# Kernel optimization log

Hardware: AMD Instinct MI355X
Metric: run time of the kernel (lower is better)

Reference implementation:

```python
import jax, jax.numpy as jnp
import numpy as np

B, T, F, H, P, HEADS = 1024, 128, 9, 256, 2048, 4
DH = H // HEADS

def _lstm_layer(x, Wih, Whh, bih, bhh):
    # x: [B,T,in]; gate order i,f,g,o (torch convention)
    xp = jnp.einsum('bti,gi->btg', x, Wih) + bih + bhh  # [B,T,4H]
    h0 = jnp.zeros((x.shape[0], Whh.shape[1]), x.dtype)
    def step(carry, xt):
        h, c = carry
        g = xt + h @ Whh.T
        i, f, gg, o = jnp.split(g, 4, axis=-1)
        c = jax.nn.sigmoid(f) * c + jax.nn.sigmoid(i) * jnp.tanh(gg)
        h = jax.nn.sigmoid(o) * jnp.tanh(c)
        return (h, c), h
    _, hs = jax.lax.scan(step, (h0, h0), jnp.swapaxes(xp, 0, 1))
    return jnp.swapaxes(hs, 0, 1)  # [B,T,H]

def _layernorm(x, g, b, eps=1e-5):
    mu = x.mean(-1, keepdims=True)
    var = ((x - mu) ** 2).mean(-1, keepdims=True)
    return (x - mu) * jax.lax.rsqrt(var + eps) * g + b

def setup_inputs():
    key = jax.random.key(0)
    ks = jax.random.split(key, 30)
    w = lambda k, s: jax.random.normal(k, s, jnp.float32) * 0.05
    return {
        'x': jax.random.normal(ks[0], (B, T, F), jnp.float32),
        'sku_indices': jnp.arange(B, dtype=jnp.int32),
        'adj': jax.random.uniform(ks[1], (P, P), jnp.float32),
        'vsn_emb_w': w(ks[2], (F, H)), 'vsn_emb_b': w(ks[3], (F, H)),
        'vsn_sel_w': w(ks[4], (F, F)), 'vsn_sel_b': w(ks[5], (F,)),
        'lstm_Wih0': w(ks[6], (4 * H, H)), 'lstm_Whh0': w(ks[7], (4 * H, H)),
        'lstm_bih0': w(ks[8], (4 * H,)), 'lstm_bhh0': w(ks[9], (4 * H,)),
        'lstm_Wih1': w(ks[10], (4 * H, H)), 'lstm_Whh1': w(ks[11], (4 * H, H)),
        'lstm_bih1': w(ks[12], (4 * H,)), 'lstm_bhh1': w(ks[13], (4 * H,)),
        'attn_in_w': w(ks[14], (3 * H, H)), 'attn_in_b': w(ks[15], (3 * H,)),
        'attn_out_w': w(ks[16], (H, H)), 'attn_out_b': w(ks[17], (H,)),
        'gnn_w': w(ks[18], (H, H)), 'gnn_b': w(ks[19], (H,)),
        'ln_g': jnp.ones((H,), jnp.float32), 'ln_b': jnp.zeros((H,), jnp.float32),
        'gate_w': w(ks[20], (H, 2 * H)), 'gate_b': w(ks[21], (H,)),
        'out_w': w(ks[22], (1, H)), 'out_b': w(ks[23], (1,)),
    }

def reference(x, sku_indices, adj, vsn_emb_w, vsn_emb_b, vsn_sel_w, vsn_sel_b,
              lstm_Wih0, lstm_Whh0, lstm_bih0, lstm_bhh0,
              lstm_Wih1, lstm_Whh1, lstm_bih1, lstm_bhh1,
              attn_in_w, attn_in_b, attn_out_w, attn_out_b,
              gnn_w, gnn_b, ln_g, ln_b, gate_w, gate_b, out_w, out_b):
    # --- TFT hidden: variable selection -> 2-layer LSTM -> MHA, take last step ---
    emb = x[..., None] * vsn_emb_w + vsn_emb_b           # [B,T,F,H]
    wts = jax.nn.softmax(x @ vsn_sel_w.T + vsn_sel_b, -1)  # [B,T,F]
    h = jnp.einsum('btf,btfh->bth', wts, emb)            # [B,T,H]
    h = _lstm_layer(h, lstm_Wih0, lstm_Whh0, lstm_bih0, lstm_bhh0)
    h = _lstm_layer(h, lstm_Wih1, lstm_Whh1, lstm_bih1, lstm_bhh1)
    qkv = h @ attn_in_w.T + attn_in_b                    # [B,T,3H]
    q, k, v = [a.reshape(B, T, HEADS, DH) for a in jnp.split(qkv, 3, axis=-1)]
    scores = jnp.einsum('bqhd,bkhd->bhqk', q, k) / np.sqrt(DH).astype(np.float32)
    attn = jax.nn.softmax(scores, -1)
    o = jnp.einsum('bhqk,bkhd->bqhd', attn, v).reshape(B, T, H)
    o = o @ attn_out_w.T + attn_out_b
    hidden = o[:, -1, :]                                  # [B,H]
    # --- GNN enrichment (all sku_indices valid here) ---
    product_embeds = jnp.zeros((P, H), hidden.dtype).at[sku_indices].set(hidden)
    degree = jnp.clip(adj.sum(1, keepdims=True), 1e-6)
    aggregated = (adj / degree) @ product_embeds          # [P,H]
    transformed = jax.nn.gelu(aggregated @ gnn_w.T + gnn_b, approximate=False)
    transformed = _layernorm(transformed, ln_g, ln_b)
    enriched = transformed[sku_indices]                   # [B,H]
    gate = jax.nn.sigmoid(jnp.concatenate([hidden, enriched], -1) @ gate_w.T + gate_b)
    combined = gate * enriched + (1.0 - gate) * hidden
    out = combined @ out_w.T + out_b                      # [B,1]
    return out.squeeze(-1)
```

## Files before the change

### kernel.cpp

```cpp
#include <hip/hip_runtime.h>
#include <hip/hip_fp16.h>

typedef _Float16 f16;
typedef _Float16 f16x8 __attribute__((ext_vector_type(8)));
typedef _Float16 f16x4 __attribute__((ext_vector_type(4)));
typedef float f32x4 __attribute__((ext_vector_type(4)));

#define B_ 1024
#define T_ 128
#define F_ 9
#define H_ 256
#define P_ 2048

#define AL(p) __hip_atomic_load((p), __ATOMIC_RELAXED, __HIP_MEMORY_SCOPE_AGENT)
#define AS(p, v) __hip_atomic_store((p), (v), __ATOMIC_RELAXED, __HIP_MEMORY_SCOPE_AGENT)

__device__ __forceinline__ float sigf(float x) { return 1.f / (1.f + __expf(-x)); }
__device__ __forceinline__ float tanh_(float x) {
  float a = fminf(fabsf(x), 12.f);
  float e = __expf(2.f * a);
  float r = 1.f - 2.f / (e + 1.f);
  return copysignf(r, x);
}

__device__ __forceinline__ f16x8 aload16(const f16* p) {
  union { unsigned long long u[2]; f16x8 v; } r;
  r.u[0] = AL((const unsigned long long*)p);
  r.u[1] = AL((const unsigned long long*)p + 1);
  return r.v;
}

__device__ __forceinline__ float blk_sum(float v) {
  __shared__ float sh[8];
  int lane = threadIdx.x & 63, w = threadIdx.x >> 6;
  int nw = blockDim.x >> 6;
#pragma unroll
  for (int o = 32; o > 0; o >>= 1) v += __shfl_xor(v, o, 64);
  __syncthreads();
  if (lane == 0) sh[w] = v;
  __syncthreads();
  float t = 0.f;
  for (int i = 0; i < nw; i++) t += sh[i];
  return t;
}

__global__ __launch_bounds__(256) void gemm_f16(
    const f16* __restrict__ A, int lda,
    const f16* __restrict__ Bt, int ldb,
    const float* __restrict__ bias,
    f16* __restrict__ o16, int ldo16,
    float* __restrict__ o32, int ldo32,
    int M, int N, int K)
{
  __shared__ __align__(16) f16 As[128][40];
  __shared__ __align__(16) f16 Bs[128][40];
  const int tid = threadIdx.x;
  const int lane = tid & 63, wave = tid >> 6;
  const int wr = (wave >> 1) * 64, wc = (wave & 1) * 64;
  const int q = lane >> 4, l15 = lane & 15;
  const int bm = blockIdx.x * 128, bn = blockIdx.y * 128;

  f32x4 acc[4][4];
#pragma unroll
  for (int i = 0; i < 4; i++)
#pragma unroll
    for (int j = 0; j < 4; j++) acc[i][j] = (f32x4){0.f, 0.f, 0.f, 0.f};

  for (int k0 = 0; k0 < K; k0 += 32) {
#pragma unroll
    for (int c = 0; c < 2; ++c) {
      int ch = tid + c * 256;
      int row = ch >> 2, kh = (ch & 3) * 8;
      *(f16x8*)&As[row][kh] = *(const f16x8*)&A[(size_t)(bm + row) * lda + k0 + kh];
      *(f16x8*)&Bs[row][kh] = *(const f16x8*)&Bt[(size_t)(bn + row) * ldb + k0 + kh];
    }
    __syncthreads();
    f16x8 af[4], bf[4];
#pragma unroll
    for (int tm = 0; tm < 4; tm++) af[tm] = *(const f16x8*)&As[wr + tm * 16 + l15][q * 8];
#pragma unroll
    for (int tn = 0; tn < 4; tn++) bf[tn] = *(const f16x8*)&Bs[wc + tn * 16 + l15][q * 8];
#pragma unroll
    for (int tm = 0; tm < 4; tm++)
#pragma unroll
      for (int tn = 0; tn < 4; tn++)
        acc[tm][tn] = __builtin_amdgcn_mfma_f32_16x16x32_f16(af[tm], bf[tn], acc[tm][tn], 0, 0, 0);
    __syncthreads();
  }
#pragma unroll
  for (int tm = 0; tm < 4; tm++) {
#pragma unroll
    for (int tn = 0; tn < 4; tn++) {
      int colg = bn + wc + tn * 16 + l15;
      float bv = bias ? bias[colg] : 0.f;
#pragma unroll
      for (int r = 0; r < 4; r++) {
        int rowg = bm + wr + tm * 16 + q * 4 + r;
        float v = acc[tm][tn][r] + bv;
        if (o32) o32[(size_t)rowg * ldo32 + colg] = v;
        if (o16) o16[(size_t)rowg * ldo16 + colg] = (f16)v;
      }
    }
  }
}

__global__ __launch_bounds__(256, 1) void lstm_pipe(
    f16* __restrict__ hio,
    const f16* __restrict__ wpk0, const f16* __restrict__ wpk1,
    const float* __restrict__ b0, const float* __restrict__ b1,
    int* __restrict__ cnt0, int* __restrict__ cnt1)
{
  __shared__ __align__(16) f16 apf[2][16][64][8];
  __shared__ __align__(16) f16 htile[32][64];
  const int tid = threadIdx.x;
  const int lane = tid & 63, w = tid >> 6;
  const int q = lane >> 4, l15 = lane & 15;
  const int layer = blockIdx.x >> 7;
  const int lbid = blockIdx.x & 127;
  const int grp = lbid & 31, s = lbid >> 5;
  const int m0 = grp * 32;
  const f16* wpk = layer ? wpk1 : wpk0;
  const float* bias = layer ? b1 : b0;
  int* myflags = (layer ? cnt1 : cnt0) + grp * 64;
  int* xflags  = cnt0 + grp * 64;

  const int own0 = ((w >> 1) == s);
  const int own1 = (((w + 4) >> 1) == s);
  const int offh = (w & 1) * 32;

  f16x8 bf[4][16];
  {
    const f16* wbase = wpk + (((size_t)(s * 4 + w) * 4) * 16) * 512 + lane * 8;
#pragma unroll
    for (int g = 0; g < 4; g++)
#pragma unroll
      for (int k = 0; k < 16; k++)
        bf[g][k] = *(const f16x8*)(wbase + (size_t)(g * 16 + k) * 512);
  }
  float bv[4];
#pragma unroll
  for (int g = 0; g < 4; g++) bv[g] = bias[g * 256 + s * 64 + w * 16 + l15];

  const int srow = lane & 15, scb = lane >> 4;
  size_t rb[2];
  rb[0] = ((size_t)(m0 + srow) * T_) * 256 + scb * 8;
  rb[1] = ((size_t)(m0 + 16 + srow) * T_) * 256 + scb * 8;

  const f16x8 zv = {(f16)0, (f16)0, (f16)0, (f16)0, (f16)0, (f16)0, (f16)0, (f16)0};

  if (layer) {
    if (tid == 0) {
      int it = 0;
      for (;;) {
        unsigned long long a = AL((unsigned long long*)xflags);
        unsigned long long b2 = AL((unsigned long long*)xflags + 1);
        if ((int)a >= 2 && (int)(a >> 32) >= 2 &&
            (int)b2 >= 2 && (int)(b2 >> 32) >= 2) break;
        __builtin_amdgcn_s_sleep(1);
        if (++it > (1 << 22)) break;
      }
    }
    __syncthreads();
  }
  f16x8 xr[2][2];
#pragma unroll
  for (int mt = 0; mt < 2; mt++) {
    if (layer) {
      xr[mt][0] = aload16(&hio[rb[mt] + (size_t)w * 32]);
      xr[mt][1] = aload16(&hio[rb[mt] + (size_t)(w + 4) * 32]);
    } else {
      xr[mt][0] = *(const f16x8*)&hio[rb[mt] + (size_t)w * 32];
      xr[mt][1] = *(const f16x8*)&hio[rb[mt] + (size_t)(w + 4) * 32];
    }
  }
  float cst[2][4] = {{0.f, 0.f, 0.f, 0.f}, {0.f, 0.f, 0.f, 0.f}};

  __syncthreads();
  if (tid == 0) AS(&myflags[s], 1);

  for (int t = 0; t < T_; ++t) {
    if (tid == 0) {
      const int needO = t + 1;
      int needX = 0;
      if (layer) { needX = t + 3; if (needX > T_ + 1) needX = T_ + 1; }
      int it = 0;
      for (;;) {
        unsigned long long a = AL((unsigned long long*)myflags);
        unsigned long long b2 = AL((unsigned long long*)myflags + 1);
        bool ok = (int)a >= needO && (int)(a >> 32) >= needO &&
                  (int)b2 >= needO && (int)(b2 >> 32) >= needO;
        if (ok && layer) {
          unsigned long long c = AL((unsigned long long*)xflags);
          unsigned long long d = AL((unsigned long long*)xflags + 1);
          ok = (int)c >= needX && (int)(c >> 32) >= needX &&
               (int)d >= needX && (int)(d >> 32) >= needX;
        }
        if (ok) break;
        __builtin_amdgcn_s_sleep(1);
        if (++it > (1 << 22)) break;
      }
    }
    __syncthreads();

#pragma unroll
    for (int mt = 0; mt < 2; mt++) {
      *(f16x8*)&apf[mt][w][lane][0]     = xr[mt][0];
      *(f16x8*)&apf[mt][w + 4][lane][0] = xr[mt][1];
      f16x8 h0 = zv, h1 = zv;
      if (t > 0) {
        if (own0) h0 = *(const f16x8*)&htile[mt * 16 + srow][offh + scb * 8];
        else      h0 = aload16(&hio[rb[mt] + (size_t)(t - 1) * 256 + (size_t)w * 32]);
        if (own1) h1 = *(const f16x8*)&htile[mt * 16 + srow][offh + scb * 8];
        else      h1 = aload16(&hio[rb[mt] + (size_t)(t - 1) * 256 + (size_t)(w + 4) * 32]);
      }
      *(f16x8*)&apf[mt][8 + w][lane][0]  = h0;
      *(f16x8*)&apf[mt][12 + w][lane][0] = h1;
    }
    __syncthreads();

    f32x4 acc[2][4];
#pragma unroll
    for (int mt = 0; mt < 2; mt++)
#pragma unroll
      for (int g = 0; g < 4; g++) acc[mt][g] = (f32x4){0.f, 0.f, 0.f, 0.f};
#pragma unroll
    for (int k = 0; k < 16; k++) {
      f16x8 a0 = *(const f16x8*)&apf[0][k][lane][0];
      f16x8 a1 = *(const f16x8*)&apf[1][k][lane][0];
#pragma unroll
      for (int g = 0; g < 4; g++) {
        acc[0][g] = __builtin_amdgcn_mfma_f32_16x16x32_f16(a0, bf[g][k], acc[0][g], 0, 0, 0);
        acc[1][g] = __builtin_amdgcn_mfma_f32_16x16x32_f16(a1, bf[g][k], acc[1][g], 0, 0, 0);
      }
    }
    if (t + 1 < T_) {
#pragma unroll
      for (int mt = 0; mt < 2; mt++) {
        if (layer) {
          xr[mt][0] = aload16(&hio[rb[mt] + (size_t)(t + 1) * 256 + (size_t)w * 32]);
          xr[mt][1] = aload16(&hio[rb[mt] + (size_t)(t + 1) * 256 + (size_t)(w + 4) * 32]);
        } else {
          xr[mt][0] = *(const f16x8*)&hio[rb[mt] + (size_t)(t + 1) * 256 + (size_t)w * 32];
          xr[mt][1] = *(const f16x8*)&hio[rb[mt] + (size_t)(t + 1) * 256 + (size_t)(w + 4) * 32];
        }
      }
    }
    f16 hn[2][4];
#pragma unroll
    for (int mt = 0; mt < 2; mt++)
#pragma unroll
      for (int r = 0; r < 4; r++) {
        float ip = acc[mt][0][r] + bv[0];
        float fp = acc[mt][1][r] + bv[1];
        float gp = acc[mt][2][r] + bv[2];
        float op = acc[mt][3][r] + bv[3];
        float cn = sigf(fp) * cst[mt][r] + sigf(ip) * tanh_(gp);
        cst[mt][r] = cn;
        hn[mt][r] = (f16)(sigf(op) * tanh_(cn));
      }
#pragma unroll
    for (int mt = 0; mt < 2; mt++)
#pragma unroll
      for (int r = 0; r < 4; r++)
        htile[mt * 16 + q * 4 + r][w * 16 + l15] = hn[mt][r];
    __syncthreads();
    {
      int row = tid >> 3, c8 = (tid & 7) * 8;
      union { unsigned long long u[2]; f16x8 v; } uh;
      uh.v = *(const f16x8*)&htile[row][c8];
      unsigned long long* dst =
          (unsigned long long*)&hio[((size_t)(m0 + row) * T_ + t) * 256 + s * 64 + c8];
      AS(dst, uh.u[0]);
      AS(dst + 1, uh.u[1]);
    }
    __syncthreads();
    if (tid == 0) AS(&myflags[s], t + 2);
  }
}

__global__ __launch_bounds__(256) void vsn_w_kernel(
    const float* __restrict__ x, const float* __restrict__ selw,
    const float* __restrict__ selb, float* __restrict__ wb)
{
  int pos = blockIdx.x * 256 + threadIdx.x;
  const float* xr = x + (size_t)pos * F_;
  float xv[F_];
#pragma unroll
  for (int f = 0; f < F_; f++) xv[f] = xr[f];
  float wv[F_]; float mx = -1e30f;
#pragma unroll
  for (int f = 0; f < F_; f++) {
    float s = selb[f];
#pragma unroll
    for (int f2 = 0; f2 < F_; f2++) s += xv[f2] * selw[f * F_ + f2];
    wv[f] = s; mx = fmaxf(mx, s);
  }
  float se = 0.f;
#pragma unroll
  for (int f = 0; f < F_; f++) { wv[f] = __expf(wv[f] - mx); se += wv[f]; }
  float inv = 1.f / se;
  float* o = wb + (size_t)pos * 18;
#pragma unroll
  for (int f = 0; f < F_; f++) {
    float wt = wv[f] * inv;
    o[f] = wt; o[9 + f] = wt * xv[f];
  }
}

__global__ __launch_bounds__(256) void vsn_h_kernel(
    const float* __restrict__ wb, const float* __restrict__ embw,
    const float* __restrict__ embb, f16* __restrict__ hout)
{
  int j = threadIdx.x;
  float ew[F_], eb[F_];
#pragma unroll
  for (int f = 0; f < F_; f++) { ew[f] = embw[f * H_ + j]; eb[f] = embb[f * H_ + j]; }
  for (int i = 0; i < 128; i++) {
    size_t pos = blockIdx.x + (size_t)i * 1024;
    const float* w = wb + pos * 18;
    float h = 0.f;
#pragma unroll
    for (int f = 0; f < F_; f++) h += w[9 + f] * ew[f] + w[f] * eb[f];
    hout[pos * H_ + j] = (f16)h;
  }
}

__global__ __launch_bounds__(256) void qk_kernel(
    const float* __restrict__ qbuf, const float* __restrict__ attn_in_w,
    float* __restrict__ qk)
{
  __shared__ float qs[256];
  int b = blockIdx.x, j = threadIdx.x;
  qs[j] = qbuf[(size_t)b * 256 + j];
  __syncthreads();
#pragma unroll
  for (int h = 0; h < 4; h++) {
    float acc = 0.f;
    for (int d = 0; d < 64; d++)
      acc += qs[h * 64 + d] * attn_in_w[(size_t)(256 + h * 64 + d) * 256 + j];
    qk[((size_t)b * 4 + h) * 256 + j] = acc * 0.125f;
  }
}

__global__ __launch_bounds__(256) void attnpool_kernel(
    const f16* __restrict__ hseq, const float* __restrict__ qk,
    float* __restrict__ hbar)
{
  __shared__ __align__(16) f16 hs[T_][264];
  __shared__ float qks[4][256];
  __shared__ float ps[4][T_];
  int b = blockIdx.x, tid = threadIdx.x;
  for (int i = tid; i < T_ * 32; i += 256) {
    int row = i >> 5, cc = (i & 31) * 8;
    *(f16x8*)&hs[row][cc] = *(const f16x8*)&hseq[((size_t)b * T_ + row) * 256 + cc];
  }
  for (int i = tid; i < 1024; i += 256) qks[i >> 8][i & 255] = qk[(size_t)b * 1024 + i];
  __syncthreads();
  if (tid < T_) {
    float s[4] = {0.f, 0.f, 0.f, 0.f};
    for (int cc = 0; cc < 32; cc++) {
      f16x8 v = *(const f16x8*)&hs[tid][cc * 8];
#pragma unroll
      for (int h = 0; h < 4; h++) {
        float a = 0.f;
#pragma unroll
        for (int j = 0; j < 8; j++) a += qks[h][cc * 8 + j] * (float)v[j];
        s[h] += a;
      }
    }
#pragma unroll
    for (int h = 0; h < 4; h++) ps[h][tid] = s[h];
  }
  __syncthreads();
  {
    int w = tid >> 6, l = tid & 63;
    float a = ps[w][l], bb = ps[w][l + 64];
    float m = fmaxf(a, bb);
#pragma unroll
    for (int o = 32; o > 0; o >>= 1) m = fmaxf(m, __shfl_xor(m, o, 64));
    float e0 = __expf(a - m), e1 = __expf(bb - m);
    float se = e0 + e1;
#pragma unroll
    for (int o = 32; o > 0; o >>= 1) se += __shfl_xor(se, o, 64);
    float inv = 1.f / se;
    ps[w][l] = e0 * inv; ps[w][l + 64] = e1 * inv;
  }
  __syncthreads();
  int j = tid;
  float acc[4] = {0.f, 0.f, 0.f, 0.f};
  for (int t = 0; t < T_; t++) {
    float hv = (float)hs[t][j];
#pragma unroll
    for (int h = 0; h < 4; h++) acc[h] += ps[h][t] * hv;
  }
#pragma unroll
  for (int h = 0; h < 4; h++) hbar[((size_t)b * 4 + h) * 256 + j] = acc[h];
}

__global__ __launch_bounds__(256) void vproj_kernel(
    const float* __restrict__ hbar, const float* __restrict__ attn_in_w,
    const float* __restrict__ attn_in_b, f16* __restrict__ aob)
{
  __shared__ float hb[4][256];
  int b = blockIdx.x, tid = threadIdx.x;
  for (int i = tid; i < 1024; i += 256) hb[i >> 8][i & 255] = hbar[(size_t)b * 1024 + i];
  __syncthreads();
  int d = tid, h = d >> 6;
  const float4* wr = (const float4*)(attn_in_w + (size_t)(512 + d) * 256);
  float acc = 0.f;
  for (int cc = 0; cc < 64; cc++) {
    float4 w4 = wr[cc];
    acc += w4.x * hb[h][cc * 4] + w4.y * hb[h][cc * 4 + 1]
         + w4.z * hb[h][cc * 4 + 2] + w4.w * hb[h][cc * 4 + 3];
  }
  aob[(size_t)b * 256 + d] = (f16)(acc + attn_in_b[512 + d]);
}

__global__ __launch_bounds__(256) void deg_adjn_kernel(
    const float* __restrict__ adj, const int* __restrict__ sku,
    f16* __restrict__ adjn)
{
  int bp = blockIdx.x;
  int p = sku[bp];
  int tid = threadIdx.x;
  float s = 0.f;
  for (int j = tid; j < P_; j += 256) s += adj[(size_t)p * P_ + j];
  float tot = blk_sum(s);
  float inv = 1.f / fmaxf(tot, 1e-6f);
  for (int b = tid; b < B_; b += 256)
    adjn[(size_t)bp * B_ + b] = (f16)(adj[(size_t)p * P_ + sku[b]] * inv);
}

__global__ void transpose_kernel(const float* __restrict__ hid, f16* __restrict__ hT)
{
  int i = blockIdx.x * 256 + threadIdx.x;
  int b = i >> 8, j = i & 255;
  hT[(size_t)j * B_ + b] = (f16)hid[i];
}

__global__ __launch_bounds__(256) void gelu_ln_kernel(
    const float* __restrict__ pre, const float* __restrict__ lg,
    const float* __restrict__ lb, float* __restrict__ enr,
    f16* __restrict__ hidcat)
{
  int row = blockIdx.x, j = threadIdx.x;
  float xv = pre[row * 256 + j];
  float ge = 0.5f * xv * (1.f + erff(xv * 0.70710678118654752f));
  float mu = blk_sum(ge) * (1.f / 256.f);
  float d = ge - mu;
  float var = blk_sum(d * d) * (1.f / 256.f);
  float y = d * rsqrtf(var + 1e-5f) * lg[j] + lb[j];
  enr[row * 256 + j] = y;
  hidcat[row * 512 + 256 + j] = (f16)y;
}

__global__ __launch_bounds__(256) void final_kernel(
    const float* __restrict__ gpre, const float* __restrict__ enr,
    const float* __restrict__ hid, const float* __restrict__ outw,
    const float* __restrict__ outb, float* __restrict__ out)
{
  int b = blockIdx.x, j = threadIdx.x;
  float gt = sigf(gpre[b * 256 + j]);
  float comb = gt * enr[b * 256 + j] + (1.f - gt) * hid[b * 256 + j];
  float v = comb * outw[j];
  float s = blk_sum(v);
  if (j == 0) out[b] = s + outb[0];
}

__global__ void prep_kernel(
    const float* Wih0, const float* Whh0, const float* Wih1, const float* Whh1,
    const float* bih0, const float* bhh0, const float* bih1, const float* bhh1,
    const float* attn_in_w, const float* attn_out_w, const float* gnn_w,
    const float* gate_w,
    f16* wpk0, f16* wpk1, f16* attninf, f16* attnoutf, f16* gnnwf, f16* gatewf,
    float* bias0, float* bias1)
{
  int idx = blockIdx.x * 256 + threadIdx.x;
  if (idx < 524288) {
    int j = idx & 7, lane = (idx >> 3) & 63, k = (idx >> 9) & 15;
    int g = (idx >> 13) & 3, w = (idx >> 15) & 3, s = (idx >> 17) & 3;
    int row = g * 256 + s * 64 + w * 16 + (lane & 15);
    int col = k * 32 + (lane >> 4) * 8 + j;
    float v0 = col < 256 ? Wih0[(size_t)row * 256 + col] : Whh0[(size_t)row * 256 + col - 256];
    float v1 = col < 256 ? Wih1[(size_t)row * 256 + col] : Whh1[(size_t)row * 256 + col - 256];
    wpk0[idx] = (f16)v0;
    wpk1[idx] = (f16)v1;
    return;
  }
  int i = idx - 524288;
  if (i < 65536) { attninf[i] = (f16)attn_in_w[i]; return; }
  i -= 65536;
  if (i < 65536) { attnoutf[i] = (f16)attn_out_w[i]; return; }
  i -= 65536;
  if (i < 65536) { gnnwf[i] = (f16)gnn_w[i]; return; }
  i -= 65536;
  if (i < 131072) { gatewf[i] = (f16)gate_w[i]; return; }
  i -= 131072;
  if (i < 1024) { bias0[i] = bih0[i] + bhh0[i]; return; }
  i -= 1024;
  if (i < 1024) { bias1[i] = bih1[i] + bhh1[i]; return; }
}

extern "C" void kernel_launch(void* const* d_in, const int* in_sizes, int n_in,
                              void* d_out, int out_size, void* d_ws, size_t ws_size,
                              hipStream_t stream)
{
  const float* x         = (const float*)d_in[0];
  const int*   sku       = (const int*)  d_in[1];
  const float* adj       = (const float*)d_in[2];
  const float* vsn_emb_w = (const float*)d_in[3];
  const float* vsn_emb_b = (const float*)d_in[4];
  const float* vsn_sel_w = (const float*)d_in[5];
  const float* vsn_sel_b = (const float*)d_in[6];
  const float* Wih0 = (const float*)d_in[7];
  const float* Whh0 = (const float*)d_in[8];
  const float* bih0 = (const float*)d_in[9];
  const float* bhh0 = (const float*)d_in[10];
  const float* Wih1 = (const float*)d_in[11];
  const float* Whh1 = (const float*)d_in[12];
  const float* bih1 = (const float*)d_in[13];
  const float* bhh1 = (const float*)d_in[14];
  const float* attn_in_w  = (const float*)d_in[15];
  const float* attn_in_b  = (const float*)d_in[16];
  const float* attn_out_w = (const float*)d_in[17];
  const float* attn_out_b = (const float*)d_in[18];
  const float* gnn_w  = (const float*)d_in[19];
  const float* gnn_b  = (const float*)d_in[20];
  const float* ln_g   = (const float*)d_in[21];
  const float* ln_b   = (const float*)d_in[22];
  const float* gate_w = (const float*)d_in[23];
  const float* gate_b = (const float*)d_in[24];
  const float* out_w  = (const float*)d_in[25];
  const float* out_b  = (const float*)d_in[26];
  (void)in_sizes; (void)n_in; (void)out_size; (void)ws_size;

  char* wsb = (char*)d_ws;
  size_t off = 0;
  auto alloc = [&](size_t bytes) -> void* {
    void* p = wsb + off;
    off += (bytes + 255) & ~(size_t)255;
    return p;
  };
  f16* hA      = (f16*)alloc((size_t)B_ * T_ * H_ * 2);
  f16* wpk0    = (f16*)alloc((size_t)1024 * 512 * 2);
  f16* wpk1    = (f16*)alloc((size_t)1024 * 512 * 2);
  f16* attninf = (f16*)alloc((size_t)256 * 256 * 2);
  f16* attnoutf= (f16*)alloc((size_t)256 * 256 * 2);
  f16* gnnwf   = (f16*)alloc((size_t)256 * 256 * 2);
  f16* gatewf  = (f16*)alloc((size_t)256 * 512 * 2);
  float* bias0 = (float*)alloc(1024 * 4);
  float* bias1 = (float*)alloc(1024 * 4);
  int* cnt0    = (int*)alloc(32 * 64 * 4);
  int* cnt1    = (int*)alloc(32 * 64 * 4);
  size_t off_tail = off;
  float* qbuf  = (float*)alloc((size_t)B_ * 256 * 4);
  float* qk    = (float*)alloc((size_t)B_ * 4 * 256 * 4);
  float* hbar  = (float*)alloc((size_t)B_ * 4 * 256 * 4);
  f16* aob     = (f16*)alloc((size_t)B_ * 256 * 2);
  float* hidden32 = (float*)alloc((size_t)B_ * 256 * 4);
  f16* hidcat  = (f16*)alloc((size_t)B_ * 512 * 2);
  f16* hT      = (f16*)alloc((size_t)256 * B_ * 2);
  f16* adjn    = (f16*)alloc((size_t)B_ * B_ * 2);
  f16* aggf    = (f16*)alloc((size_t)B_ * 256 * 2);
  float* gnnpre= (float*)alloc((size_t)B_ * 256 * 4);
  float* enr32 = (float*)alloc((size_t)B_ * 256 * 4);
  float* gatepre=(float*)alloc((size_t)B_ * 256 * 4);
  float* wb    = (float*)(wsb + off_tail);

  hipMemsetAsync(cnt0, 0, 2 * 32 * 64 * 4, stream);

  prep_kernel<<<3336, 256, 0, stream>>>(
      Wih0, Whh0, Wih1, Whh1, bih0, bhh0, bih1, bhh1,
      attn_in_w, attn_out_w, gnn_w, gate_w,
      wpk0, wpk1, attninf, attnoutf, gnnwf, gatewf, bias0, bias1);

  vsn_w_kernel<<<512, 256, 0, stream>>>(x, vsn_sel_w, vsn_sel_b, wb);
  vsn_h_kernel<<<1024, 256, 0, stream>>>(wb, vsn_emb_w, vsn_emb_b, hA);
  lstm_pipe<<<256, 256, 0, stream>>>(hA, wpk0, wpk1, bias0, bias1, cnt0, cnt1);

  dim3 gS(B_ / 128, 256 / 128);
  gemm_f16<<<gS, 256, 0, stream>>>(hA + (size_t)(T_ - 1) * 256, T_ * 256, attninf, 256,
                                   attn_in_b, nullptr, 0, qbuf, 256, B_, 256, 256);
  qk_kernel<<<B_, 256, 0, stream>>>(qbuf, attn_in_w, qk);
  attnpool_kernel<<<B_, 256, 0, stream>>>(hA, qk, hbar);
  vproj_kernel<<<B_, 256, 0, stream>>>(hbar, attn_in_w, attn_in_b, aob);
  gemm_f16<<<gS, 256, 0, stream>>>(aob, 256, attnoutf, 256, attn_out_b,
                                   hidcat, 512, hidden32, 256, B_, 256, 256);
  deg_adjn_kernel<<<B_, 256, 0, stream>>>(adj, sku, adjn);
  transpose_kernel<<<B_, 256, 0, stream>>>(hidden32, hT);
  gemm_f16<<<gS, 256, 0, stream>>>(adjn, 1024, hT, 1024, nullptr,
                                   aggf, 256, nullptr, 0, B_, 256, 1024);
  gemm_f16<<<gS, 256, 0, stream>>>(aggf, 256, gnnwf, 256, gnn_b,
                                   nullptr, 0, gnnpre, 256, B_, 256, 256);
  gelu_ln_kernel<<<B_, 256, 0, stream>>>(gnnpre, ln_g, ln_b, enr32, hidcat);
  gemm_f16<<<gS, 256, 0, stream>>>(hidcat, 512, gatewf, 512, gate_b,
                                   nullptr, 0, gatepre, 256, B_, 256, 512);
  final_kernel<<<B_, 256, 0, stream>>>(gatepre, enr32, hidden32, out_w, out_b, (float*)d_out);
}
```

Measured before the change: 1.015 ms.

## Fuse attention pooling kernels, emit transposed output from GEMM, fold flag reset

Merges qk_kernel, attnpool_kernel and vproj_kernel into one attn_fused_kernel, so the qk and hbar intermediates stay in shared memory instead of going through global memory. The attn-out GEMM epilogue now also writes a transposed f16 copy, which replaces the separate transpose kernel. The hipMemsetAsync for the LSTM sync counters is folded into prep_kernel. The aim is fewer launches and less global traffic in the post-LSTM tail. The trade-offs are uncoalesced transposed stores in the GEMM epilogue and higher per-block shared memory use in the fused kernel.

```diff
diff --git a/kernel.cpp b/kernel.cpp
--- a/kernel.cpp
+++ b/kernel.cpp
@@ -12,6 +12,7 @@
 #define H_ 256
 #define P_ 2048
 
+typedef unsigned long long ull;
 #define AL(p) __hip_atomic_load((p), __ATOMIC_RELAXED, __HIP_MEMORY_SCOPE_AGENT)
 #define AS(p, v) __hip_atomic_store((p), (v), __ATOMIC_RELAXED, __HIP_MEMORY_SCOPE_AGENT)
 
@@ -24,9 +25,9 @@
 }
 
 __device__ __forceinline__ f16x8 aload16(const f16* p) {
-  union { unsigned long long u[2]; f16x8 v; } r;
-  r.u[0] = AL((const unsigned long long*)p);
-  r.u[1] = AL((const unsigned long long*)p + 1);
+  union { ull u[2]; f16x8 v; } r;
+  r.u[0] = AL((const ull*)p);
+  r.u[1] = AL((const ull*)p + 1);
   return r.v;
 }
 
@@ -50,6 +51,7 @@
     const float* __restrict__ bias,
     f16* __restrict__ o16, int ldo16,
     float* __restrict__ o32, int ldo32,
+    f16* __restrict__ o16t, int ldt,
     int M, int N, int K)
 {
   __shared__ __align__(16) f16 As[128][40];
@@ -99,6 +101,7 @@
         float v = acc[tm][tn][r] + bv;
         if (o32) o32[(size_t)rowg * ldo32 + colg] = v;
         if (o16) o16[(size_t)rowg * ldo16 + colg] = (f16)v;
+        if (o16t) o16t[(size_t)colg * ldt + rowg] = (f16)v;
       }
     }
   }
@@ -152,8 +155,8 @@
     if (tid == 0) {
       int it = 0;
       for (;;) {
-        unsigned long long a = AL((unsigned long long*)xflags);
-        unsigned long long b2 = AL((unsigned long long*)xflags + 1);
+        ull a = AL((ull*)xflags);
+        ull b2 = AL((ull*)xflags + 1);
         if ((int)a >= 2 && (int)(a >> 32) >= 2 &&
             (int)b2 >= 2 && (int)(b2 >> 32) >= 2) break;
         __builtin_amdgcn_s_sleep(1);
@@ -185,13 +188,13 @@
       if (layer) { needX = t + 3; if (needX > T_ + 1) needX = T_ + 1; }
       int it = 0;
       for (;;) {
-        unsigned long long a = AL((unsigned long long*)myflags);
-        unsigned long long b2 = AL((unsigned long long*)myflags + 1);
+        ull a = AL((ull*)myflags);
+        ull b2 = AL((ull*)myflags + 1);
         bool ok = (int)a >= needO && (int)(a >> 32) >= needO &&
                   (int)b2 >= needO && (int)(b2 >> 32) >= needO;
         if (ok && layer) {
-          unsigned long long c = AL((unsigned long long*)xflags);
-          unsigned long long d = AL((unsigned long long*)xflags + 1);
+          ull c = AL((ull*)xflags);
+          ull d = AL((ull*)xflags + 1);
           ok = (int)c >= needX && (int)(c >> 32) >= needX &&
                (int)d >= needX && (int)(d >> 32) >= needX;
         }
@@ -266,10 +269,10 @@
     __syncthreads();
     {
       int row = tid >> 3, c8 = (tid & 7) * 8;
-      union { unsigned long long u[2]; f16x8 v; } uh;
+      union { ull u[2]; f16x8 v; } uh;
       uh.v = *(const f16x8*)&htile[row][c8];
-      unsigned long long* dst =
-          (unsigned long long*)&hio[((size_t)(m0 + row) * T_ + t) * 256 + s * 64 + c8];
+      ull* dst =
+          (ull*)&hio[((size_t)(m0 + row) * T_ + t) * 256 + s * 64 + c8];
       AS(dst, uh.u[0]);
       AS(dst + 1, uh.u[1]);
     }
@@ -325,36 +328,33 @@
   }
 }
 
-__global__ __launch_bounds__(256) void qk_kernel(
-    const float* __restrict__ qbuf, const float* __restrict__ attn_in_w,
-    float* __restrict__ qk)
-{
+__global__ __launch_bounds__(256) void attn_fused_kernel(
+    const f16* __restrict__ hseq, const float* __restrict__ qbuf,
+    const float* __restrict__ attn_in_w, const float* __restrict__ attn_in_b,
+    f16* __restrict__ aob)
+{
+  __shared__ __align__(16) f16 hs[T_][264];
   __shared__ float qs[256];
-  int b = blockIdx.x, j = threadIdx.x;
-  qs[j] = qbuf[(size_t)b * 256 + j];
-  __syncthreads();
-#pragma unroll
-  for (int h = 0; h < 4; h++) {
-    float acc = 0.f;
-    for (int d = 0; d < 64; d++)
-      acc += qs[h * 64 + d] * attn_in_w[(size_t)(256 + h * 64 + d) * 256 + j];
-    qk[((size_t)b * 4 + h) * 256 + j] = acc * 0.125f;
-  }
-}
-
-__global__ __launch_bounds__(256) void attnpool_kernel(
-    const f16* __restrict__ hseq, const float* __restrict__ qk,
-    float* __restrict__ hbar)
-{
-  __shared__ __align__(16) f16 hs[T_][264];
   __shared__ float qks[4][256];
   __shared__ float ps[4][T_];
+  __shared__ float hb[4][256];
   int b = blockIdx.x, tid = threadIdx.x;
   for (int i = tid; i < T_ * 32; i += 256) {
     int row = i >> 5, cc = (i & 31) * 8;
     *(f16x8*)&hs[row][cc] = *(const f16x8*)&hseq[((size_t)b * T_ + row) * 256 + cc];
   }
-  for (int i = tid; i < 1024; i += 256) qks[i >> 8][i & 255] = qk[(size_t)b * 1024 + i];
+  qs[tid] = qbuf[(size_t)b * 256 + tid];
+  __syncthreads();
+  {
+    int j = tid;
+#pragma unroll
+    for (int h = 0; h < 4; h++) {
+      float acc = 0.f;
+      for (int d = 0; d < 64; d++)
+        acc += qs[h * 64 + d] * attn_in_w[(size_t)(256 + h * 64 + d) * 256 + j];
+      qks[h][j] = acc * 0.125f;
+    }
+  }
   __syncthreads();
   if (tid < T_) {
     float s[4] = {0.f, 0.f, 0.f, 0.f};
@@ -386,34 +386,29 @@
     ps[w][l] = e0 * inv; ps[w][l + 64] = e1 * inv;
   }
   __syncthreads();
-  int j = tid;
-  float acc[4] = {0.f, 0.f, 0.f, 0.f};
-  for (int t = 0; t < T_; t++) {
-    float hv = (float)hs[t][j];
-#pragma unroll
-    for (int h = 0; h < 4; h++) acc[h] += ps[h][t] * hv;
-  }
-#pragma unroll
-  for (int h = 0; h < 4; h++) hbar[((size_t)b * 4 + h) * 256 + j] = acc[h];
-}
-
-__global__ __launch_bounds__(256) void vproj_kernel(
-    const float* __restrict__ hbar, const float* __restrict__ attn_in_w,
-    const float* __restrict__ attn_in_b, f16* __restrict__ aob)
-{
-  __shared__ float hb[4][256];
-  int b = blockIdx.x, tid = threadIdx.x;
-  for (int i = tid; i < 1024; i += 256) hb[i >> 8][i & 255] = hbar[(size_t)b * 1024 + i];
-  __syncthreads();
-  int d = tid, h = d >> 6;
-  const float4* wr = (const float4*)(attn_in_w + (size_t)(512 + d) * 256);
-  float acc = 0.f;
-  for (int cc = 0; cc < 64; cc++) {
-    float4 w4 = wr[cc];
-    acc += w4.x * hb[h][cc * 4] + w4.y * hb[h][cc * 4 + 1]
-         + w4.z * hb[h][cc * 4 + 2] + w4.w * hb[h][cc * 4 + 3];
-  }
-  aob[(size_t)b * 256 + d] = (f16)(acc + attn_in_b[512 + d]);
+  {
+    int j = tid;
+    float acc[4] = {0.f, 0.f, 0.f, 0.f};
+    for (int t = 0; t < T_; t++) {
+      float hv = (float)hs[t][j];
+#pragma unroll
+      for (int h = 0; h < 4; h++) acc[h] += ps[h][t] * hv;
+    }
+#pragma unroll
+    for (int h = 0; h < 4; h++) hb[h][j] = acc[h];
+  }
+  __syncthreads();
+  {
+    int d = tid, h = d >> 6;
+    const float4* wr = (const float4*)(attn_in_w + (size_t)(512 + d) * 256);
+    float acc = 0.f;
+    for (int cc = 0; cc < 64; cc++) {
+      float4 w4 = wr[cc];
+      acc += w4.x * hb[h][cc * 4] + w4.y * hb[h][cc * 4 + 1]
+           + w4.z * hb[h][cc * 4 + 2] + w4.w * hb[h][cc * 4 + 3];
+    }
+    aob[(size_t)b * 256 + d] = (f16)(acc + attn_in_b[512 + d]);
+  }
 }
 
 __global__ __launch_bounds__(256) void deg_adjn_kernel(
@@ -431,13 +426,6 @@
     adjn[(size_t)bp * B_ + b] = (f16)(adj[(size_t)p * P_ + sku[b]] * inv);
 }
 
-__global__ void transpose_kernel(const float* __restrict__ hid, f16* __restrict__ hT)
-{
-  int i = blockIdx.x * 256 + threadIdx.x;
-  int b = i >> 8, j = i & 255;
-  hT[(size_t)j * B_ + b] = (f16)hid[i];
-}
-
 __global__ __launch_bounds__(256) void gelu_ln_kernel(
     const float* __restrict__ pre, const float* __restrict__ lg,
     const float* __restrict__ lb, float* __restrict__ enr,
@@ -473,7 +461,7 @@
     const float* attn_in_w, const float* attn_out_w, const float* gnn_w,
     const float* gate_w,
     f16* wpk0, f16* wpk1, f16* attninf, f16* attnoutf, f16* gnnwf, f16* gatewf,
-    float* bias0, float* bias1)
+    float* bias0, float* bias1, int* flagz)
 {
   int idx = blockIdx.x * 256 + threadIdx.x;
   if (idx < 524288) {
@@ -499,6 +487,8 @@
   if (i < 1024) { bias0[i] = bih0[i] + bhh0[i]; return; }
   i -= 1024;
   if (i < 1024) { bias1[i] = bih1[i] + bhh1[i]; return; }
+  i -= 1024;
+  if (i < 4096) { flagz[i] = 0; return; }
 }
 
 extern "C" void kernel_launch(void* const* d_in, const int* in_sizes, int n_in,
@@ -554,8 +544,6 @@
   int* cnt1    = (int*)alloc(32 * 64 * 4);
   size_t off_tail = off;
   float* qbuf  = (float*)alloc((size_t)B_ * 256 * 4);
-  float* qk    = (float*)alloc((size_t)B_ * 4 * 256 * 4);
-  float* hbar  = (float*)alloc((size_t)B_ * 4 * 256 * 4);
   f16* aob     = (f16*)alloc((size_t)B_ * 256 * 2);
   float* hidden32 = (float*)alloc((size_t)B_ * 256 * 4);
   f16* hidcat  = (f16*)alloc((size_t)B_ * 512 * 2);
@@ -567,12 +555,10 @@
   float* gatepre=(float*)alloc((size_t)B_ * 256 * 4);
   float* wb    = (float*)(wsb + off_tail);
 
-  hipMemsetAsync(cnt0, 0, 2 * 32 * 64 * 4, stream);
-
-  prep_kernel<<<3336, 256, 0, stream>>>(
+  prep_kernel<<<3353, 256, 0, stream>>>(
       Wih0, Whh0, Wih1, Whh1, bih0, bhh0, bih1, bhh1,
       attn_in_w, attn_out_w, gnn_w, gate_w,
-      wpk0, wpk1, attninf, attnoutf, gnnwf, gatewf, bias0, bias1);
+      wpk0, wpk1, attninf, attnoutf, gnnwf, gatewf, bias0, bias1, cnt0);
 
   vsn_w_kernel<<<512, 256, 0, stream>>>(x, vsn_sel_w, vsn_sel_b, wb);
   vsn_h_kernel<<<1024, 256, 0, stream>>>(wb, vsn_emb_w, vsn_emb_b, hA);
@@ -580,20 +566,22 @@
 
   dim3 gS(B_ / 128, 256 / 128);
   gemm_f16<<<gS, 256, 0, stream>>>(hA + (size_t)(T_ - 1) * 256, T_ * 256, attninf, 256,
-                                   attn_in_b, nullptr, 0, qbuf, 256, B_, 256, 256);
-  qk_kernel<<<B_, 256, 0, stream>>>(qbuf, attn_in_w, qk);
-  attnpool_kernel<<<B_, 256, 0, stream>>>(hA, qk, hbar);
-  vproj_kernel<<<B_, 256, 0, stream>>>(hbar, attn_in_w, attn_in_b, aob);
+                                   attn_in_b, nullptr, 0, qbuf, 256, nullptr, 0,
+                                   B_, 256, 256);
+  attn_fused_kernel<<<B_, 256, 0, stream>>>(hA, qbuf, attn_in_w, attn_in_b, aob);
   gemm_f16<<<gS, 256, 0, stream>>>(aob, 256, attnoutf, 256, attn_out_b,
-                                   hidcat, 512, hidden32, 256, B_, 256, 256);
+                                   hidcat, 512, hidden32, 256, hT, B_,
+                                   B_, 256, 256);
   deg_adjn_kernel<<<B_, 256, 0, stream>>>(adj, sku, adjn);
-  transpose_kernel<<<B_, 256, 0, stream>>>(hidden32, hT);
   gemm_f16<<<gS, 256, 0, stream>>>(adjn, 1024, hT, 1024, nullptr,
-                                   aggf, 256, nullptr, 0, B_, 256, 1024);
+                                   aggf, 256, nullptr, 0, nullptr, 0,
+                                   B_, 256, 1024);
   gemm_f16<<<gS, 256, 0, stream>>>(aggf, 256, gnnwf, 256, gnn_b,
-                                   nullptr, 0, gnnpre, 256, B_, 256, 256);
+                                   nullptr, 0, gnnpre, 256, nullptr, 0,
+                                   B_, 256, 256);
   gelu_ln_kernel<<<B_, 256, 0, stream>>>(gnnpre, ln_g, ln_b, enr32, hidcat);
   gemm_f16<<<gS, 256, 0, stream>>>(hidcat, 512, gatewf, 512, gate_b,
-                                   nullptr, 0, gatepre, 256, B_, 256, 512);
+                                   nullptr, 0, gatepre, 256, nullptr, 0,
+                                   B_, 256, 512);
   final_kernel<<<B_, 256, 0, stream>>>(gatepre, enr32, hidden32, out_w, out_b, (float*)d_out);
 }
```

Result: no change. 998.7 us (-1.6%).
